# Optimization experiments

Hardware: AMD Instinct MI355X
Metric: run time of the kernel (lower is better)

The kernel has to match this reference:

```python
import jax, jax.numpy as jnp
import numpy as np

MARGIN = 1.0

def setup_inputs() -> dict:
    key = jax.random.key(0)
    k1, k2 = jax.random.split(key)
    B, D, NUM_CLASSES = 4096, 512, 64
    inputs = jax.random.normal(k1, (B, D), dtype=jnp.float32)
    labels = jax.random.randint(k2, (B,), 0, NUM_CLASSES, dtype=jnp.int64)
    return {"inputs": inputs, "labels": labels}

def reference(inputs, labels):
    # Full pairwise squared L2 distances via the ||a-b||^2 = ||a||^2 + ||b||^2 - 2 a.b expansion
    sq = jnp.sum(inputs * inputs, axis=1)                      # [B]
    d2 = sq[:, None] + sq[None, :] - 2.0 * (inputs @ inputs.T)  # [B, B]
    d2 = jnp.maximum(d2, 0.0)
    # Safe sqrt: zero (self) distances get exactly 0 without NaN-producing sqrt(0) grads
    nz = d2 > 1e-12
    dist = jnp.where(nz, jnp.sqrt(jnp.where(nz, d2, 1.0)), 0.0)  # [B, B]

    mask = labels[:, None] == labels[None, :]                   # [B, B] same-class mask (includes self)
    mask_f = mask.astype(dist.dtype)

    # Per-anchor: mean distance to positives (self included, contributing 0, as in the torch loop)
    ap_mean = jnp.sum(dist * mask_f, axis=1) / jnp.sum(mask_f, axis=1)  # [B]
    # Per-anchor: min distance to negatives
    an_min = jnp.min(jnp.where(mask, jnp.inf, dist), axis=1)            # [B]

    tmp = ap_mean - an_min + MARGIN                             # [B]
    # `if tmp > 0: loss += tmp` over the batch == sum of relu(tmp)
    return jnp.sum(jnp.maximum(tmp, 0.0))
```

## Files before the change

### kernel.cpp

```cpp
#include <hip/hip_runtime.h>
#include <hip/hip_bf16.h>

typedef unsigned short u16;
typedef unsigned int u32;
typedef __attribute__((ext_vector_type(8))) short short8;
typedef __attribute__((ext_vector_type(8))) u16 ushort8;
typedef __attribute__((ext_vector_type(4))) float f32x4;

#define B_SZ 4096
#define D_SZ 512
#define NCLS 64
#define BK   32
#define NKK  (D_SZ / BK)
#define NT   32
#define NBLK (NT * (NT + 1) / 2)
#define TILE_ELEMS (128 * BK)

#define WAITV4()  asm volatile("s_waitcnt vmcnt(4)" ::: "memory")
#define WAITV0()  asm volatile("s_waitcnt vmcnt(0)" ::: "memory")
#define BARRIER() asm volatile("s_barrier" ::: "memory")


__device__ __forceinline__ u16 f2bf(float x) {
    union { float f; u32 u; } a; a.f = x;
    u32 r = a.u + 0x7fffu + ((a.u >> 16) & 1u);
    return (u16)(r >> 16);
}

__device__ __forceinline__ void gload16(const void* g, void* l) {
    __builtin_amdgcn_global_load_lds(
        (const __attribute__((address_space(1))) u32*)g,
        (__attribute__((address_space(3))) u32*)l,
        16, 0, 0);
}

__device__ __forceinline__ void stage_tile32(const u16* __restrict__ gsrc, u16* dst, int t) {
    #pragma unroll
    for (int q = 0; q < 2; ++q) {
        const int s = t + q * 256;
        const int r = s >> 2;
        const int col = ((s & 3) ^ (r & 3)) << 3;
        gload16(gsrc + (size_t)r * D_SZ + col, dst + s * 8);
    }
}


__global__ __launch_bounds__(256) void prep_kernel(
    const float* __restrict__ in, u16* __restrict__ bfout,
    float* __restrict__ sq, float* __restrict__ ap_sum, u32* __restrict__ an_min)
{
    const int wave = threadIdx.x >> 6, l = threadIdx.x & 63;
    const int row = blockIdx.x * 4 + wave;
    const float* p = in + (size_t)row * D_SZ + l * 8;
    float4 v0 = *(const float4*)p;
    float4 v1 = *(const float4*)(p + 4);
    float s = v0.x*v0.x + v0.y*v0.y + v0.z*v0.z + v0.w*v0.w
            + v1.x*v1.x + v1.y*v1.y + v1.z*v1.z + v1.w*v1.w;
    ushort8 o;
    o[0]=f2bf(v0.x); o[1]=f2bf(v0.y); o[2]=f2bf(v0.z); o[3]=f2bf(v0.w);
    o[4]=f2bf(v1.x); o[5]=f2bf(v1.y); o[6]=f2bf(v1.z); o[7]=f2bf(v1.w);
    *(ushort8*)(bfout + (size_t)row * D_SZ + l * 8) = o;
    #pragma unroll
    for (int off = 1; off < 64; off <<= 1) s += __shfl_xor(s, off);
    if (l == 0) {
        sq[row] = s;
        ap_sum[row] = 0.0f;
        an_min[row] = 0x7f800000u;
    }
}


__global__ __launch_bounds__(256) void tile_kernel(
    const u16* __restrict__ bfin, const int* __restrict__ lab,
    const float* __restrict__ sq, float* __restrict__ ap_sum, u32* __restrict__ an_min)
{
    __shared__ u16 As[3][TILE_ELEMS];
    __shared__ u16 Bs[3][TILE_ELEMS];
    __shared__ float sqA[128], sqB[128];
    __shared__ int labA[128], labB[128];

    const int t = threadIdx.x;

    int bid = blockIdx.x;
    bid = (bid & 7) * (NBLK / 8) + (bid >> 3);

    int tm = (int)((__builtin_sqrtf(8.0f * (float)bid + 1.0f) - 1.0f) * 0.5f);
    while ((tm + 1) * (tm + 2) / 2 <= bid) ++tm;
    while (tm * (tm + 1) / 2 > bid) --tm;
    const int tn = bid - tm * (tm + 1) / 2;
    const bool diag = (tm == tn);

    const int rowBase = tm * 128;
    const int colBase = tn * 128;

    if (t < 128) { labA[t] = lab[rowBase + t]; sqA[t] = sq[rowBase + t]; }
    else { int u = t - 128; labB[u] = lab[colBase + u]; sqB[u] = sq[colBase + u]; }

    const int wave = t >> 6, lane = t & 63;
    const int wr = wave >> 1, wc = wave & 1;
    const int g = lane >> 4, c = lane & 15;

    f32x4 acc[4][4];
    #pragma unroll
    for (int i = 0; i < 4; ++i)
        #pragma unroll
        for (int j = 0; j < 4; ++j)
            acc[i][j] = (f32x4){0.f, 0.f, 0.f, 0.f};

    const u16* gA = bfin + (size_t)rowBase * D_SZ;
    const u16* gB = bfin + (size_t)colBase * D_SZ;

    __syncthreads();

    stage_tile32(gA,      As[0], t);
    stage_tile32(gB,      Bs[0], t);
    stage_tile32(gA + BK, As[1], t);
    stage_tile32(gB + BK, Bs[1], t);

    const int sw = (g ^ (c & 3)) << 3;

    #pragma unroll
    for (int kk = 0; kk < NKK; ++kk) {
        if (kk < NKK - 1) { WAITV4(); }
        else              { WAITV0(); }
        BARRIER();

        if (kk + 2 < NKK) {
            stage_tile32(gA + (kk + 2) * BK, As[(kk + 2) % 3], t);
            stage_tile32(gB + (kk + 2) * BK, Bs[(kk + 2) % 3], t);
        }

        const u16* abuf = As[kk % 3];
        const u16* bbuf = Bs[kk % 3];

        short8 a[4], b[4];
        #pragma unroll
        for (int mi = 0; mi < 4; ++mi)
            a[mi] = *(const short8*)&abuf[(wr * 64 + mi * 16 + c) * BK + sw];
        #pragma unroll
        for (int ni = 0; ni < 4; ++ni)
            b[ni] = *(const short8*)&bbuf[(wc * 64 + ni * 16 + c) * BK + sw];

        #pragma unroll
        for (int mi = 0; mi < 4; ++mi)
            #pragma unroll
            for (int ni = 0; ni < 4; ++ni)
                acc[mi][ni] = __builtin_amdgcn_mfma_f32_16x16x32_bf16(a[mi], b[ni], acc[mi][ni], 0, 0, 0);
    }

    float sc[4], mc[4];
    #pragma unroll
    for (int ni = 0; ni < 4; ++ni) { sc[ni] = 0.0f; mc[ni] = __builtin_inff(); }

    #pragma unroll
    for (int mi = 0; mi < 4; ++mi) {
        #pragma unroll
        for (int r = 0; r < 4; ++r) {
            const int lrow = wr * 64 + mi * 16 + g * 4 + r;
            const int i = rowBase + lrow;
            const int li = labA[lrow];
            const float sqi = sqA[lrow];
            float s = 0.0f;
            float mn = __builtin_inff();
            #pragma unroll
            for (int ni = 0; ni < 4; ++ni) {
                const int lcol = wc * 64 + ni * 16 + c;
                float d2 = sqi + sqB[lcol] - 2.0f * acc[mi][ni][r];
                d2 = fmaxf(d2, 0.0f);
                float dist = (d2 > 1e-12f) ? __builtin_sqrtf(d2) : 0.0f;
                if (diag && lrow == lcol) dist = 0.0f;
                if (li == labB[lcol]) { s += dist; sc[ni] += dist; }
                else                  { mn = fminf(mn, dist); mc[ni] = fminf(mc[ni], dist); }
            }
            #pragma unroll
            for (int off = 1; off < 16; off <<= 1) {
                s += __shfl_xor(s, off);
                mn = fminf(mn, __shfl_xor(mn, off));
            }
            if (c == 0) {
                atomicAdd(&ap_sum[i], s);
                atomicMin(&an_min[i], __float_as_uint(mn));
            }
        }
    }

    if (!diag) {
        #pragma unroll
        for (int ni = 0; ni < 4; ++ni) {
            float s = sc[ni], mn = mc[ni];
            s += __shfl_xor(s, 16); s += __shfl_xor(s, 32);
            mn = fminf(mn, __shfl_xor(mn, 16)); mn = fminf(mn, __shfl_xor(mn, 32));
            if (lane < 16) {
                const int j = colBase + wc * 64 + ni * 16 + c;
                atomicAdd(&ap_sum[j], s);
                atomicMin(&an_min[j], __float_as_uint(mn));
            }
        }
    }
}


__global__ __launch_bounds__(1024) void final_kernel(
    const float* __restrict__ ap_sum, const u32* __restrict__ an_min,
    const int* __restrict__ lab, float* __restrict__ out)
{
    __shared__ int cnt[NCLS];
    __shared__ float wsum[16];
    const int t = threadIdx.x;
    if (t < NCLS) cnt[t] = 0;
    __syncthreads();
    for (int i = t; i < B_SZ; i += 1024) atomicAdd(&cnt[lab[i]], 1);
    __syncthreads();
    float v = 0.0f;
    for (int i = t; i < B_SZ; i += 1024) {
        float apm = ap_sum[i] / (float)cnt[lab[i]];
        float anm = __uint_as_float(an_min[i]);
        v += fmaxf(apm - anm + 1.0f, 0.0f);
    }
    #pragma unroll
    for (int off = 1; off < 64; off <<= 1) v += __shfl_xor(v, off);
    if ((t & 63) == 0) wsum[t >> 6] = v;
    __syncthreads();
    if (t == 0) {
        float s = 0.0f;
        #pragma unroll
        for (int w = 0; w < 16; ++w) s += wsum[w];
        out[0] = s;
    }
}


extern "C" void kernel_launch(void* const* d_in, const int* in_sizes, int n_in,
                              void* d_out, int out_size, void* d_ws, size_t ws_size,
                              hipStream_t stream) {
    const float* inputs = (const float*)d_in[0];
    const int* labels = (const int*)d_in[1];
    float* out = (float*)d_out;

    char* ws = (char*)d_ws;
    float* ap_sum = (float*)ws;
    u32* an_min = (u32*)(ws + 16384);
    float* sq = (float*)(ws + 32768);
    u16* bfin = (u16*)(ws + 65536);

    prep_kernel<<<dim3(B_SZ / 4), dim3(256), 0, stream>>>(inputs, bfin, sq, ap_sum, an_min);
    tile_kernel<<<dim3(NBLK), dim3(256), 0, stream>>>(bfin, labels, sq, ap_sum, an_min);
    final_kernel<<<dim3(1), dim3(1024), 0, stream>>>(ap_sum, an_min, labels, out);
}
```

Measured before the change: 40.13 us.

## Replace global atomics with per-tile partial buffers and a deterministic two-stage reduction

```diff
diff --git a/kernel.cpp b/kernel.cpp
--- a/kernel.cpp
+++ b/kernel.cpp
@@ -46,8 +46,7 @@
 
 
 __global__ __launch_bounds__(256) void prep_kernel(
-    const float* __restrict__ in, u16* __restrict__ bfout,
-    float* __restrict__ sq, float* __restrict__ ap_sum, u32* __restrict__ an_min)
+    const float* __restrict__ in, u16* __restrict__ bfout, float* __restrict__ sq)
 {
     const int wave = threadIdx.x >> 6, l = threadIdx.x & 63;
     const int row = blockIdx.x * 4 + wave;
@@ -62,17 +61,15 @@
     *(ushort8*)(bfout + (size_t)row * D_SZ + l * 8) = o;
     #pragma unroll
     for (int off = 1; off < 64; off <<= 1) s += __shfl_xor(s, off);
-    if (l == 0) {
-        sq[row] = s;
-        ap_sum[row] = 0.0f;
-        an_min[row] = 0x7f800000u;
-    }
+    if (l == 0) sq[row] = s;
 }
 
 
 __global__ __launch_bounds__(256) void tile_kernel(
     const u16* __restrict__ bfin, const int* __restrict__ lab,
-    const float* __restrict__ sq, float* __restrict__ ap_sum, u32* __restrict__ an_min)
+    const float* __restrict__ sq,
+    float* __restrict__ pr_sum, float* __restrict__ pr_min,
+    float* __restrict__ pc_sum, float* __restrict__ pc_min)
 {
     __shared__ u16 As[3][TILE_ELEMS];
     __shared__ u16 Bs[3][TILE_ELEMS];
@@ -157,7 +154,6 @@
         #pragma unroll
         for (int r = 0; r < 4; ++r) {
             const int lrow = wr * 64 + mi * 16 + g * 4 + r;
-            const int i = rowBase + lrow;
             const int li = labA[lrow];
             const float sqi = sqA[lrow];
             float s = 0.0f;
@@ -178,8 +174,9 @@
                 mn = fminf(mn, __shfl_xor(mn, off));
             }
             if (c == 0) {
-                atomicAdd(&ap_sum[i], s);
-                atomicMin(&an_min[i], __float_as_uint(mn));
+                const int slot = (bid * 2 + wc) * 128 + lrow;
+                pr_sum[slot] = s;
+                pr_min[slot] = mn;
             }
         }
     }
@@ -191,40 +188,63 @@
             s += __shfl_xor(s, 16); s += __shfl_xor(s, 32);
             mn = fminf(mn, __shfl_xor(mn, 16)); mn = fminf(mn, __shfl_xor(mn, 32));
             if (lane < 16) {
-                const int j = colBase + wc * 64 + ni * 16 + c;
-                atomicAdd(&ap_sum[j], s);
-                atomicMin(&an_min[j], __float_as_uint(mn));
+                const int col = wc * 64 + ni * 16 + c;
+                const int slot = (bid * 2 + wr) * 128 + col;
+                pc_sum[slot] = s;
+                pc_min[slot] = mn;
             }
         }
     }
 }
 
 
-__global__ __launch_bounds__(1024) void final_kernel(
-    const float* __restrict__ ap_sum, const u32* __restrict__ an_min,
-    const int* __restrict__ lab, float* __restrict__ out)
+__global__ __launch_bounds__(256) void final1_kernel(
+    const float* __restrict__ pr_sum, const float* __restrict__ pr_min,
+    const float* __restrict__ pc_sum, const float* __restrict__ pc_min,
+    const int* __restrict__ lab, float* __restrict__ bsum)
 {
     __shared__ int cnt[NCLS];
-    __shared__ float wsum[16];
+    __shared__ float wsum[4];
     const int t = threadIdx.x;
     if (t < NCLS) cnt[t] = 0;
     __syncthreads();
-    for (int i = t; i < B_SZ; i += 1024) atomicAdd(&cnt[lab[i]], 1);
-    __syncthreads();
-    float v = 0.0f;
-    for (int i = t; i < B_SZ; i += 1024) {
-        float apm = ap_sum[i] / (float)cnt[lab[i]];
-        float anm = __uint_as_float(an_min[i]);
-        v += fmaxf(apm - anm + 1.0f, 0.0f);
-    }
+    for (int i = t; i < B_SZ; i += 256) atomicAdd(&cnt[lab[i]], 1);
+    __syncthreads();
+
+    const int i = blockIdx.x * 256 + t;
+    const int tmb = i >> 7, lrow = i & 127;
+    float s = 0.0f, mn = __builtin_inff();
+
+    const int base = tmb * (tmb + 1) / 2;
+    for (int tn = 0; tn <= tmb; ++tn) {
+        const int bid = base + tn;
+        s += pr_sum[(bid * 2 + 0) * 128 + lrow] + pr_sum[(bid * 2 + 1) * 128 + lrow];
+        mn = fminf(mn, fminf(pr_min[(bid * 2 + 0) * 128 + lrow],
+                             pr_min[(bid * 2 + 1) * 128 + lrow]));
+    }
+    for (int tp = tmb + 1; tp < NT; ++tp) {
+        const int bid = tp * (tp + 1) / 2 + tmb;
+        s += pc_sum[(bid * 2 + 0) * 128 + lrow] + pc_sum[(bid * 2 + 1) * 128 + lrow];
+        mn = fminf(mn, fminf(pc_min[(bid * 2 + 0) * 128 + lrow],
+                             pc_min[(bid * 2 + 1) * 128 + lrow]));
+    }
+
+    const float apm = s / (float)cnt[lab[i]];
+    float v = fmaxf(apm - mn + 1.0f, 0.0f);
+
     #pragma unroll
     for (int off = 1; off < 64; off <<= 1) v += __shfl_xor(v, off);
     if ((t & 63) == 0) wsum[t >> 6] = v;
     __syncthreads();
-    if (t == 0) {
+    if (t == 0) bsum[blockIdx.x] = wsum[0] + wsum[1] + wsum[2] + wsum[3];
+}
+
+
+__global__ void final2_kernel(const float* __restrict__ bsum, float* __restrict__ out) {
+    if (threadIdx.x == 0) {
         float s = 0.0f;
         #pragma unroll
-        for (int w = 0; w < 16; ++w) s += wsum[w];
+        for (int k = 0; k < 16; ++k) s += bsum[k];
         out[0] = s;
     }
 }
@@ -238,12 +258,18 @@
     float* out = (float*)d_out;
 
     char* ws = (char*)d_ws;
-    float* ap_sum = (float*)ws;
-    u32* an_min = (u32*)(ws + 16384);
-    float* sq = (float*)(ws + 32768);
-    u16* bfin = (u16*)(ws + 65536);
-
-    prep_kernel<<<dim3(B_SZ / 4), dim3(256), 0, stream>>>(inputs, bfin, sq, ap_sum, an_min);
-    tile_kernel<<<dim3(NBLK), dim3(256), 0, stream>>>(bfin, labels, sq, ap_sum, an_min);
-    final_kernel<<<dim3(1), dim3(1024), 0, stream>>>(ap_sum, an_min, labels, out);
-}
+    float* sq     = (float*)(ws);
+    float* pr_sum = (float*)(ws + 0x010000);
+    float* pr_min = (float*)(ws + 0x0A0000);
+    float* pc_sum = (float*)(ws + 0x130000);
+    float* pc_min = (float*)(ws + 0x1C0000);
+    float* bsum   = (float*)(ws + 0x250000);
+    u16*   bfin   = (u16*)  (ws + 0x260000);
+
+    prep_kernel<<<dim3(B_SZ / 4), dim3(256), 0, stream>>>(inputs, bfin, sq);
+    tile_kernel<<<dim3(NBLK), dim3(256), 0, stream>>>(bfin, labels, sq,
+                                                      pr_sum, pr_min, pc_sum, pc_min);
+    final1_kernel<<<dim3(16), dim3(256), 0, stream>>>(pr_sum, pr_min, pc_sum, pc_min,
+                                                      labels, bsum);
+    final2_kernel<<<dim3(1), dim3(64), 0, stream>>>(bsum, out);
+}
```

Result: slower. 53.16 us (+32.5%).

## Switch Gram matrix GEMM from bf16 to fp8 e4m3 MFMA

Applied to the files above, without the earlier changes.

```diff
diff --git a/kernel.cpp b/kernel.cpp
--- a/kernel.cpp
+++ b/kernel.cpp
@@ -1,30 +1,36 @@
 #include <hip/hip_runtime.h>
 #include <hip/hip_bf16.h>
 
+typedef unsigned char u8;
 typedef unsigned short u16;
 typedef unsigned int u32;
-typedef __attribute__((ext_vector_type(8))) short short8;
-typedef __attribute__((ext_vector_type(8))) u16 ushort8;
+typedef unsigned long long u64;
 typedef __attribute__((ext_vector_type(4))) float f32x4;
 
 #define B_SZ 4096
 #define D_SZ 512
 #define NCLS 64
-#define BK   32
+#define BK   64
 #define NKK  (D_SZ / BK)
 #define NT   32
 #define NBLK (NT * (NT + 1) / 2)
-#define TILE_ELEMS (128 * BK)
+#define TILE_BYTES (128 * BK)
 
 #define WAITV4()  asm volatile("s_waitcnt vmcnt(4)" ::: "memory")
 #define WAITV0()  asm volatile("s_waitcnt vmcnt(0)" ::: "memory")
 #define BARRIER() asm volatile("s_barrier" ::: "memory")
 
 
-__device__ __forceinline__ u16 f2bf(float x) {
+__device__ __forceinline__ u8 f2fp8(float x) {
     union { float f; u32 u; } a; a.f = x;
-    u32 r = a.u + 0x7fffu + ((a.u >> 16) & 1u);
-    return (u16)(r >> 16);
+    u32 s = (a.u >> 24) & 0x80u;
+    u32 m = a.u & 0x7fffffffu;
+    u32 r = m + 0x7ffffu + ((m >> 20) & 1u);
+    int e = (int)(r >> 23) - 127 + 7;
+    u32 mant = (r >> 20) & 7u;
+    if (e <= 0) return (u8)s;
+    if (e >= 16) return (u8)(s | 0x7Eu);
+    return (u8)(s | ((u32)e << 3) | mant);
 }
 
 __device__ __forceinline__ void gload16(const void* g, void* l) {
@@ -34,19 +40,19 @@
         16, 0, 0);
 }
 
-__device__ __forceinline__ void stage_tile32(const u16* __restrict__ gsrc, u16* dst, int t) {
+__device__ __forceinline__ void stage_fp8(const u8* __restrict__ gsrc, u8* dst, int t) {
     #pragma unroll
     for (int q = 0; q < 2; ++q) {
         const int s = t + q * 256;
         const int r = s >> 2;
-        const int col = ((s & 3) ^ (r & 3)) << 3;
-        gload16(gsrc + (size_t)r * D_SZ + col, dst + s * 8);
+        const int c16 = (s & 3) ^ (r & 3);
+        gload16(gsrc + (size_t)r * D_SZ + (c16 << 4), dst + s * 16);
     }
 }
 
 
 __global__ __launch_bounds__(256) void prep_kernel(
-    const float* __restrict__ in, u16* __restrict__ bfout,
+    const float* __restrict__ in, u8* __restrict__ bf8,
     float* __restrict__ sq, float* __restrict__ ap_sum, u32* __restrict__ an_min)
 {
     const int wave = threadIdx.x >> 6, l = threadIdx.x & 63;
@@ -56,10 +62,15 @@
     float4 v1 = *(const float4*)(p + 4);
     float s = v0.x*v0.x + v0.y*v0.y + v0.z*v0.z + v0.w*v0.w
             + v1.x*v1.x + v1.y*v1.y + v1.z*v1.z + v1.w*v1.w;
-    ushort8 o;
-    o[0]=f2bf(v0.x); o[1]=f2bf(v0.y); o[2]=f2bf(v0.z); o[3]=f2bf(v0.w);
-    o[4]=f2bf(v1.x); o[5]=f2bf(v1.y); o[6]=f2bf(v1.z); o[7]=f2bf(v1.w);
-    *(ushort8*)(bfout + (size_t)row * D_SZ + l * 8) = o;
+    u64 pk =  (u64)f2fp8(v0.x)
+           | ((u64)f2fp8(v0.y) << 8)
+           | ((u64)f2fp8(v0.z) << 16)
+           | ((u64)f2fp8(v0.w) << 24)
+           | ((u64)f2fp8(v1.x) << 32)
+           | ((u64)f2fp8(v1.y) << 40)
+           | ((u64)f2fp8(v1.z) << 48)
+           | ((u64)f2fp8(v1.w) << 56);
+    *(u64*)(bf8 + (size_t)row * D_SZ + l * 8) = pk;
     #pragma unroll
     for (int off = 1; off < 64; off <<= 1) s += __shfl_xor(s, off);
     if (l == 0) {
@@ -71,11 +82,11 @@
 
 
 __global__ __launch_bounds__(256) void tile_kernel(
-    const u16* __restrict__ bfin, const int* __restrict__ lab,
+    const u8* __restrict__ bf8, const int* __restrict__ lab,
     const float* __restrict__ sq, float* __restrict__ ap_sum, u32* __restrict__ an_min)
 {
-    __shared__ u16 As[3][TILE_ELEMS];
-    __shared__ u16 Bs[3][TILE_ELEMS];
+    __shared__ u8 As[3][TILE_BYTES];
+    __shared__ u8 Bs[3][TILE_BYTES];
     __shared__ float sqA[128], sqB[128];
     __shared__ int labA[128], labB[128];
 
@@ -107,17 +118,17 @@
         for (int j = 0; j < 4; ++j)
             acc[i][j] = (f32x4){0.f, 0.f, 0.f, 0.f};
 
-    const u16* gA = bfin + (size_t)rowBase * D_SZ;
-    const u16* gB = bfin + (size_t)colBase * D_SZ;
-
-    __syncthreads();
-
-    stage_tile32(gA,      As[0], t);
-    stage_tile32(gB,      Bs[0], t);
-    stage_tile32(gA + BK, As[1], t);
-    stage_tile32(gB + BK, Bs[1], t);
-
-    const int sw = (g ^ (c & 3)) << 3;
+    const u8* gA = bf8 + (size_t)rowBase * D_SZ;
+    const u8* gB = bf8 + (size_t)colBase * D_SZ;
+
+    __syncthreads();
+
+    stage_fp8(gA,      As[0], t);
+    stage_fp8(gB,      Bs[0], t);
+    stage_fp8(gA + BK, As[1], t);
+    stage_fp8(gB + BK, Bs[1], t);
+
+    const int x3 = c & 3, sub = (g & 1) * 8, gh = g >> 1;
 
     #pragma unroll
     for (int kk = 0; kk < NKK; ++kk) {
@@ -126,26 +137,29 @@
         BARRIER();
 
         if (kk + 2 < NKK) {
-            stage_tile32(gA + (kk + 2) * BK, As[(kk + 2) % 3], t);
-            stage_tile32(gB + (kk + 2) * BK, Bs[(kk + 2) % 3], t);
-        }
-
-        const u16* abuf = As[kk % 3];
-        const u16* bbuf = Bs[kk % 3];
-
-        short8 a[4], b[4];
-        #pragma unroll
-        for (int mi = 0; mi < 4; ++mi)
-            a[mi] = *(const short8*)&abuf[(wr * 64 + mi * 16 + c) * BK + sw];
-        #pragma unroll
-        for (int ni = 0; ni < 4; ++ni)
-            b[ni] = *(const short8*)&bbuf[(wc * 64 + ni * 16 + c) * BK + sw];
-
-        #pragma unroll
-        for (int mi = 0; mi < 4; ++mi)
+            stage_fp8(gA + (kk + 2) * BK, As[(kk + 2) % 3], t);
+            stage_fp8(gB + (kk + 2) * BK, Bs[(kk + 2) % 3], t);
+        }
+
+        const u8* abuf = As[kk % 3];
+        const u8* bbuf = Bs[kk % 3];
+
+        #pragma unroll
+        for (int ks = 0; ks < 2; ++ks) {
+            const int koff = (((ks * 2 + gh) ^ x3) << 4) + sub;
+            long a[4], b[4];
+            #pragma unroll
+            for (int mi = 0; mi < 4; ++mi)
+                a[mi] = *(const long*)(abuf + (wr * 64 + mi * 16 + c) * BK + koff);
             #pragma unroll
             for (int ni = 0; ni < 4; ++ni)
-                acc[mi][ni] = __builtin_amdgcn_mfma_f32_16x16x32_bf16(a[mi], b[ni], acc[mi][ni], 0, 0, 0);
+                b[ni] = *(const long*)(bbuf + (wc * 64 + ni * 16 + c) * BK + koff);
+            #pragma unroll
+            for (int mi = 0; mi < 4; ++mi)
+                #pragma unroll
+                for (int ni = 0; ni < 4; ++ni)
+                    acc[mi][ni] = __builtin_amdgcn_mfma_f32_16x16x32_fp8_fp8(a[mi], b[ni], acc[mi][ni], 0, 0, 0);
+        }
     }
 
     float sc[4], mc[4];
@@ -241,9 +255,9 @@
     float* ap_sum = (float*)ws;
     u32* an_min = (u32*)(ws + 16384);
     float* sq = (float*)(ws + 32768);
-    u16* bfin = (u16*)(ws + 65536);
-
-    prep_kernel<<<dim3(B_SZ / 4), dim3(256), 0, stream>>>(inputs, bfin, sq, ap_sum, an_min);
-    tile_kernel<<<dim3(NBLK), dim3(256), 0, stream>>>(bfin, labels, sq, ap_sum, an_min);
+    u8* bf8 = (u8*)(ws + 65536);
+
+    prep_kernel<<<dim3(B_SZ / 4), dim3(256), 0, stream>>>(inputs, bf8, sq, ap_sum, an_min);
+    tile_kernel<<<dim3(NBLK), dim3(256), 0, stream>>>(bf8, labels, sq, ap_sum, an_min);
     final_kernel<<<dim3(1), dim3(1024), 0, stream>>>(ap_sum, an_min, labels, out);
 }
```

After: 39.53 us, median of 3. No clear change (-1.5%).
